# Performance work log

Measured on AMD Instinct MI355X. Metric: run time of the kernel, lower is better.

The kernel has to match this reference:

```python
import jax, jax.numpy as jnp
import numpy as np

G, N, D, K, OUT = 2048, 64, 128, 128, 10  # K*D == input_dim == 16384

def setup_inputs() -> dict:
    key = jax.random.key(0)
    k1, k2, k3, k4, k5 = jax.random.split(key, 5)
    x = jax.random.normal(k1, (G, N, D), dtype=jnp.float32)
    # nn.Linear(node_dim, input_dim/node_dim): weight [K, D], bias [K]
    W_att = jax.random.normal(k2, (K, D), dtype=jnp.float32) * (1.0 / np.sqrt(D))
    b_att = jax.random.normal(k3, (K,), dtype=jnp.float32) * 0.01
    # nn.Linear(input_dim, output_dim): weight [OUT, K*D], bias [OUT]
    W1 = jax.random.normal(k4, (OUT, K * D), dtype=jnp.float32) * (1.0 / np.sqrt(K * D))
    b1 = jax.random.normal(k5, (OUT,), dtype=jnp.float32) * 0.01
    return {"x": x, "W_att": W_att, "b_att": b_att, "W1": W1, "b1": b1}

def reference(x, W_att, b_att, W1, b1):
    # Per-graph gram matrix X^T X : [G, D, D], quantized to 2 decimals
    gram = jnp.einsum('gnd,gne->gde', x, x)
    gram = jnp.round(gram * 100.0) / 100.0
    # attend: Linear(D -> K) applied row-wise to gram -> attn_coef [G, D, K]
    attn = jnp.einsum('gde,ke->gdk', gram, W_att) + b_att
    # attn_weights = attn^T ([G, K, D]); pooled = attn_weights @ gram -> [G, K, D]
    pooled = jnp.einsum('gdk,gde->gke', attn, gram)
    flat = pooled.reshape(x.shape[0], K * D)  # view(input_dim)
    # linear1 (dropout omitted: eval mode)
    return flat @ W1.T + b1
```

## Files before the change

kernel.cpp:

```cpp
#include <hip/hip_runtime.h>

typedef __attribute__((ext_vector_type(8)))  __bf16    bf16x8;
typedef __attribute__((ext_vector_type(4)))  __bf16    bf16x4;
typedef __attribute__((ext_vector_type(16))) float     f32x16;
typedef __attribute__((ext_vector_type(4)))  _Float16  f16x4;
typedef __attribute__((ext_vector_type(2)))  __fp16    h16x2;
typedef __attribute__((ext_vector_type(8)))  __fp16    h16x8;

constexpr int NG  = 2048;
constexpr int NN  = 64;
constexpr int DD  = 128;
constexpr int KK  = 128;
constexpr int OUTD = 10;

__device__ __host__ inline void tileOf(int t, int& ti, int& tj) {
    if (t < 4)      { ti = 0; tj = t;     }
    else if (t < 7) { ti = 1; tj = t - 3; }
    else if (t < 9) { ti = 2; tj = t - 5; }
    else            { ti = 3; tj = 3;     }
}

__device__ inline int xtIdx(int r, int c) { return r * 64  + (c ^ ((r & 7) << 3)); }
__device__ inline int gIdx (int r, int c) { return r * 128 + (c ^ ((r & 15) << 3)); }

#if __has_builtin(__builtin_amdgcn_fdot2)
__device__ __forceinline__ float dot2f(h16x2 a, h16x2 b, float c) {
    return __builtin_amdgcn_fdot2(a, b, c, false);
}
#else
__device__ __forceinline__ float dot2f(h16x2 a, h16x2 b, float c) {
    return c + (float)a[0] * (float)b[0] + (float)a[1] * (float)b[1];
}
#endif

__global__ __launch_bounds__(128)
void precompute_kernel(const float* __restrict__ Wa,
                       const float* __restrict__ b_att,
                       const float* __restrict__ W1,
                       float* __restrict__ A,
                       float* __restrict__ c)
{
    const int o = blockIdx.x >> 7;
    const int f = blockIdx.x & 127;
    const int e = threadIdx.x;
    const float* __restrict__ W1o = W1 + (size_t)o * (KK * DD);

    float acc = 0.f, cacc = 0.f;
    for (int k = 0; k < KK; ++k) {
        const float w1 = W1o[k * DD + e];
        acc  += Wa[k * DD + f] * w1;
        cacc += b_att[k] * w1;
    }
    A[((size_t)o * DD + f) * DD + e] = acc;
    if (f == 0) c[o * DD + e] = cacc;
}

__global__ __launch_bounds__(256)
void pack_kernel(const float* __restrict__ A, _Float16* __restrict__ Sp)
{
    const int b = blockIdx.x;
    const int o = b / 10, t = b - o * 10;
    int ti, tj; tileOf(t, ti, tj);
    const int l  = threadIdx.x & 63;
    const int rq = threadIdx.x >> 6;
    const int e  = tj * 32 + (l & 31);
    const float* __restrict__ Ao = A + (size_t)o * DD * DD;

    f16x4 p;
#pragma unroll
    for (int j = 0; j < 4; ++j) {
        const int f = ti * 32 + j + 8 * rq + 4 * (l >> 5);
        float v;
        if (f < e)       v = Ao[f * DD + e] + Ao[e * DD + f];
        else if (f == e) v = Ao[f * DD + f];
        else             v = 0.f;
        p[j] = (_Float16)v;
    }
    *(f16x4*)&Sp[(size_t)((o * 10 + t) * 64 + l) * 16 + rq * 4] = p;
}

__device__ __forceinline__ void process_graph(
    const float* __restrict__ xg,
    __bf16* __restrict__ XtL, __bf16* __restrict__ GL,
    float (*__restrict__ sp)[DD], float* __restrict__ sOut,
    int tid, int w, int l, int l31, int l5, int extraBase,
    f32x16& hacc0, f32x16& haccX)
{
    {
        const int f = tid & 127, half = tid >> 7;
#pragma unroll
        for (int ch = 0; ch < 2; ++ch) {
            float v[8];
#pragma unroll
            for (int i = 0; i < 8; ++i) v[i] = xg[(half * 16 + ch * 8 + i) * DD + f];
            bf16x8 p;
#pragma unroll
            for (int i = 0; i < 8; ++i) p[i] = (__bf16)v[i];
            *(bf16x8*)&XtL[xtIdx(f, half * 16 + ch * 8)] = p;
        }
    }
    __syncthreads();

    const int ti  = w & 3;
    const int tj0 = (w >> 2) * 2;
    f32x16 acc0, acc1;
#pragma unroll
    for (int i = 0; i < 16; ++i) { acc0[i] = 0.f; acc1[i] = 0.f; }
    {
        const int arow  = ti  * 32 + l31;
        const int brow0 = tj0 * 32 + l31;
#pragma unroll
        for (int ks = 0; ks < 4; ++ks) {
            const int kc = ks * 16 + l5 * 8;
            bf16x8 a  = *(const bf16x8*)&XtL[xtIdx(arow, kc)];
            bf16x8 b0 = *(const bf16x8*)&XtL[xtIdx(brow0, kc)];
            bf16x8 b1 = *(const bf16x8*)&XtL[xtIdx(brow0 + 32, kc)];
            acc0 = __builtin_amdgcn_mfma_f32_32x32x16_bf16(a, b0, acc0, 0, 0, 0);
            acc1 = __builtin_amdgcn_mfma_f32_32x32x16_bf16(a, b1, acc1, 0, 0, 0);
        }
    }
    __syncthreads();

    {
        float sum0 = 0.f, sum1 = 0.f;
#pragma unroll
        for (int tt = 0; tt < 2; ++tt) {
            const int e = (tj0 + tt) * 32 + l31;
#pragma unroll
            for (int g2 = 0; g2 < 4; ++g2) {
                bf16x4 p;
#pragma unroll
                for (int j = 0; j < 4; ++j) {
                    const float av = tt ? acc1[g2 * 4 + j] : acc0[g2 * 4 + j];
                    const float q = rintf(av * 100.f) * 0.01f;
                    p[j] = (__bf16)q;
                    if (tt) sum1 += q; else sum0 += q;
                }
                const int fbase = ti * 32 + g2 * 8 + l5 * 4;
                *(bf16x4*)&GL[gIdx(e, fbase)] = p;
            }
        }
        sp[ti * 2 + l5][tj0 * 32 + l31]       = sum0;
        sp[ti * 2 + l5][(tj0 + 1) * 32 + l31] = sum1;
    }
    __syncthreads();

    if (w == 2 || w == 3) {
        const int e = (w - 2) * 64 + l;
        float s = 0.f;
#pragma unroll
        for (int i = 0; i < 8; ++i) s += sp[i][e];
        sOut[e] = s;
    }

#pragma unroll
    for (int i = 0; i < 16; ++i) hacc0[i] = 0.f;
    {
        int hti, htj; tileOf(w, hti, htj);
        const int ra = hti * 32 + l31, rb = htj * 32 + l31;
#pragma unroll
        for (int ks = 0; ks < 8; ++ks) {
            const int kc = ks * 16 + l5 * 8;
            bf16x8 a = *(const bf16x8*)&GL[gIdx(ra, kc)];
            bf16x8 b = *(const bf16x8*)&GL[gIdx(rb, kc)];
            hacc0 = __builtin_amdgcn_mfma_f32_32x32x16_bf16(a, b, hacc0, 0, 0, 0);
        }
    }
    if (w == extraBase || w == extraBase + 1) {
        int ti1, tj1; tileOf(8 + (w - extraBase), ti1, tj1);
        const int ra = ti1 * 32 + l31, rb = tj1 * 32 + l31;
#pragma unroll
        for (int ks = 0; ks < 8; ++ks) {
            const int kc = ks * 16 + l5 * 8;
            bf16x8 a = *(const bf16x8*)&GL[gIdx(ra, kc)];
            bf16x8 b = *(const bf16x8*)&GL[gIdx(rb, kc)];
            haccX = __builtin_amdgcn_mfma_f32_32x32x16_bf16(a, b, haccX, 0, 0, 0);
        }
    }
    __syncthreads();
}

__global__ __launch_bounds__(512)
void graph_kernel(const float* __restrict__ x,
                  const _Float16* __restrict__ Sp,
                  const float* __restrict__ cg,
                  const float* __restrict__ bias1,
                  float* __restrict__ out)
{
    __shared__ __align__(16) char ldsraw[20 * 512 * 4];
    __shared__ float sp[8][DD];
    __shared__ float sA[DD], sB[DD];

    __bf16* const XtL = (__bf16*)ldsraw;
    __bf16* const GL  = (__bf16*)ldsraw;
    float*  const PP  = (float*)ldsraw;

    const int g0  = blockIdx.x * 2;
    const int g1  = g0 + 1;
    const int tid = threadIdx.x;
    const int w   = tid >> 6;
    const int l   = tid & 63;
    const int l31 = l & 31;
    const int l5  = l >> 5;

    f32x16 hA0, hB0, hX1;
#pragma unroll
    for (int i = 0; i < 16; ++i) hX1[i] = 0.f;

    process_graph(x + (size_t)g0 * NN * DD, XtL, GL, sp, sA,
                  tid, w, l, l31, l5, 6, hA0, hX1);
    process_graph(x + (size_t)g1 * NN * DD, XtL, GL, sp, sB,
                  tid, w, l, l31, l5, 4, hB0, hX1);

    h16x2 hA[8], hB[8], hX[8];
#pragma unroll
    for (int i = 0; i < 8; ++i) {
        hA[i] = __builtin_amdgcn_cvt_pkrtz(hA0[2 * i], hA0[2 * i + 1]);
        hB[i] = __builtin_amdgcn_cvt_pkrtz(hB0[2 * i], hB0[2 * i + 1]);
        hX[i] = __builtin_amdgcn_cvt_pkrtz(hX1[2 * i], hX1[2 * i + 1]);
    }

#pragma unroll
    for (int o = 0; o < OUTD; ++o) {
        const _Float16* __restrict__ spp = Sp + (size_t)((o * 10 + w) * 64 + l) * 16;
        const h16x8 s0 = *(const h16x8*)&spp[0];
        const h16x8 s1 = *(const h16x8*)&spp[8];
        float tA = 0.f, tB = 0.f;
#pragma unroll
        for (int i = 0; i < 4; ++i) {
            const h16x2 p = { s0[2 * i], s0[2 * i + 1] };
            tA = dot2f(p, hA[i], tA);
            tB = dot2f(p, hB[i], tB);
        }
#pragma unroll
        for (int i = 0; i < 4; ++i) {
            const h16x2 p = { s1[2 * i], s1[2 * i + 1] };
            tA = dot2f(p, hA[4 + i], tA);
            tB = dot2f(p, hB[4 + i], tB);
        }
        if (w >= 4) {
            const _Float16* __restrict__ sp2 =
                Sp + (size_t)((o * 10 + 8 + (w & 1)) * 64 + l) * 16;
            const h16x8 e0 = *(const h16x8*)&sp2[0];
            const h16x8 e1 = *(const h16x8*)&sp2[8];
            float tx = 0.f;
#pragma unroll
            for (int i = 0; i < 4; ++i) {
                const h16x2 p = { e0[2 * i], e0[2 * i + 1] };
                tx = dot2f(p, hX[i], tx);
            }
#pragma unroll
            for (int i = 0; i < 4; ++i) {
                const h16x2 p = { e1[2 * i], e1[2 * i + 1] };
                tx = dot2f(p, hX[4 + i], tx);
            }
            if (w >= 6) tA += tx; else tB += tx;
        }
        if (w == 0) {
            tA += cg[o * DD + l] * sA[l] + cg[o * DD + 64 + l] * sA[64 + l];
            tB += cg[o * DD + l] * sB[l] + cg[o * DD + 64 + l] * sB[64 + l];
        }
        PP[o * 512 + tid]        = tA;
        PP[(10 + o) * 512 + tid] = tB;
    }
    __syncthreads();

    for (int p = w; p < 2 * OUTD; p += 8) {
        const float4 q0 = *(const float4*)&PP[p * 512 + l * 8];
        const float4 q1 = *(const float4*)&PP[p * 512 + l * 8 + 4];
        float v = (q0.x + q0.y) + (q0.z + q0.w) + (q1.x + q1.y) + (q1.z + q1.w);
        v += __shfl_down(v, 32, 64);
        v += __shfl_down(v, 16, 64);
        v += __shfl_down(v, 8, 64);
        v += __shfl_down(v, 4, 64);
        v += __shfl_down(v, 2, 64);
        v += __shfl_down(v, 1, 64);
        if (l == 0) {
            const int gg = (p < OUTD) ? g0 : g1;
            const int oo = (p < OUTD) ? p : p - OUTD;
            out[(size_t)gg * OUTD + oo] = v + bias1[oo];
        }
    }
}

extern "C" void kernel_launch(void* const* d_in, const int* in_sizes, int n_in,
                              void* d_out, int out_size, void* d_ws, size_t ws_size,
                              hipStream_t stream)
{
    const float* x     = (const float*)d_in[0];
    const float* Wa    = (const float*)d_in[1];
    const float* b_att = (const float*)d_in[2];
    const float* W1    = (const float*)d_in[3];
    const float* bias1 = (const float*)d_in[4];
    float* out = (float*)d_out;

    float*    A  = (float*)d_ws;
    float*    c  = A + (size_t)OUTD * DD * DD;
    _Float16* Sp = (_Float16*)(c + OUTD * DD);

    precompute_kernel<<<OUTD * DD, 128, 0, stream>>>(Wa, b_att, W1, A, c);
    pack_kernel<<<100, 256, 0, stream>>>(A, Sp);
    graph_kernel<<<NG / 2, 512, 0, stream>>>(x, Sp, c, bias1, out);
}
```

Baseline: 48.63 us.

## Fuse weight precompute and fp16 pack into one tiled LDS kernel

After: 43.23 us. 11.1% less time.

```diff
diff --git a/kernel.cpp b/kernel.cpp
--- a/kernel.cpp
+++ b/kernel.cpp
@@ -33,50 +33,81 @@
 }
 #endif
 
-__global__ __launch_bounds__(128)
-void precompute_kernel(const float* __restrict__ Wa,
-                       const float* __restrict__ b_att,
-                       const float* __restrict__ W1,
-                       float* __restrict__ A,
-                       float* __restrict__ c)
+__global__ __launch_bounds__(256)
+void fused_sp_kernel(const float* __restrict__ Wa,
+                     const float* __restrict__ b_att,
+                     const float* __restrict__ W1,
+                     _Float16* __restrict__ Sp,
+                     float* __restrict__ cgout)
 {
-    const int o = blockIdx.x >> 7;
-    const int f = blockIdx.x & 127;
-    const int e = threadIdx.x;
+    const int blk = blockIdx.x;
+    const int o = blk / 10, t = blk - o * 10;
+    int ti, tj; tileOf(t, ti, tj);
+    const int Fi = ti * 32, Ej = tj * 32;
     const float* __restrict__ W1o = W1 + (size_t)o * (KK * DD);
 
-    float acc = 0.f, cacc = 0.f;
-    for (int k = 0; k < KK; ++k) {
-        const float w1 = W1o[k * DD + e];
-        acc  += Wa[k * DD + f] * w1;
-        cacc += b_att[k] * w1;
-    }
-    A[((size_t)o * DD + f) * DD + e] = acc;
-    if (f == 0) c[o * DD + e] = cacc;
-}
-
-__global__ __launch_bounds__(256)
-void pack_kernel(const float* __restrict__ A, _Float16* __restrict__ Sp)
-{
-    const int b = blockIdx.x;
-    const int o = b / 10, t = b - o * 10;
-    int ti, tj; tileOf(t, ti, tj);
-    const int l  = threadIdx.x & 63;
-    const int rq = threadIdx.x >> 6;
-    const int e  = tj * 32 + (l & 31);
-    const float* __restrict__ Ao = A + (size_t)o * DD * DD;
-
-    f16x4 p;
-#pragma unroll
-    for (int j = 0; j < 4; ++j) {
-        const int f = ti * 32 + j + 8 * rq + 4 * (l >> 5);
-        float v;
-        if (f < e)       v = Ao[f * DD + e] + Ao[e * DD + f];
-        else if (f == e) v = Ao[f * DD + f];
-        else             v = 0.f;
-        p[j] = (_Float16)v;
-    }
-    *(f16x4*)&Sp[(size_t)((o * 10 + t) * 64 + l) * 16 + rq * 4] = p;
+    __shared__ float WaF[KK][32];
+    __shared__ float WaE[KK][32];
+    __shared__ float W1F[KK][32];
+    __shared__ float W1E[KK][32];
+    __shared__ float AFE[32][33];
+    __shared__ float AEF[32][33];
+    __shared__ float bsh[KK];
+
+    const int tid = threadIdx.x;
+
+    for (int r0 = 0; r0 < KK; r0 += 8) {
+        const int r = r0 + (tid >> 5), cc = tid & 31;
+        WaF[r][cc] = Wa[r * DD + Fi + cc];
+        WaE[r][cc] = Wa[r * DD + Ej + cc];
+        W1F[r][cc] = W1o[r * DD + Fi + cc];
+        W1E[r][cc] = W1o[r * DD + Ej + cc];
+    }
+    if (tid < KK) bsh[tid] = b_att[tid];
+    __syncthreads();
+
+    {
+        const int rloc = tid >> 3;
+        const int q    = (tid & 7) * 4;
+        float a0 = 0.f, a1 = 0.f, a2 = 0.f, a3 = 0.f;
+        float b0 = 0.f, b1 = 0.f, b2 = 0.f, b3 = 0.f;
+        for (int k = 0; k < KK; ++k) {
+            const float av = WaF[k][rloc];
+            const float4 wv = *(const float4*)&W1E[k][q];
+            a0 += av * wv.x; a1 += av * wv.y; a2 += av * wv.z; a3 += av * wv.w;
+            const float bv = WaE[k][rloc];
+            const float4 vv = *(const float4*)&W1F[k][q];
+            b0 += bv * vv.x; b1 += bv * vv.y; b2 += bv * vv.z; b3 += bv * vv.w;
+        }
+        AFE[rloc][q] = a0; AFE[rloc][q + 1] = a1; AFE[rloc][q + 2] = a2; AFE[rloc][q + 3] = a3;
+        AEF[rloc][q] = b0; AEF[rloc][q + 1] = b1; AEF[rloc][q + 2] = b2; AEF[rloc][q + 3] = b3;
+    }
+    __syncthreads();
+
+    {
+        const int l  = tid & 63;
+        const int rq = tid >> 6;
+        const int eg = l & 31;
+        const int e  = Ej + eg;
+        f16x4 p;
+#pragma unroll
+        for (int j = 0; j < 4; ++j) {
+            const int fl = j + 8 * rq + 4 * (l >> 5);
+            const int f  = Fi + fl;
+            float v;
+            if (f < e)       v = AFE[fl][eg] + AEF[eg][fl];
+            else if (f == e) v = AFE[fl][eg];
+            else             v = 0.f;
+            p[j] = (_Float16)v;
+        }
+        *(f16x4*)&Sp[(size_t)((o * 10 + t) * 64 + l) * 16 + rq * 4] = p;
+    }
+
+    if (ti == 0 && tid < 32) {
+        float s = 0.f;
+        for (int k = 0; k < KK; ++k) s += bsh[k] * W1E[k][tid];
+        cgout[o * DD + Ej + tid] = s;
+    }
 }
 
 __device__ __forceinline__ void process_graph(
@@ -294,11 +325,9 @@
     const float* bias1 = (const float*)d_in[4];
     float* out = (float*)d_out;
 
-    float*    A  = (float*)d_ws;
-    float*    c  = A + (size_t)OUTD * DD * DD;
-    _Float16* Sp = (_Float16*)(c + OUTD * DD);
-
-    precompute_kernel<<<OUTD * DD, 128, 0, stream>>>(Wa, b_att, W1, A, c);
-    pack_kernel<<<100, 256, 0, stream>>>(A, Sp);
-    graph_kernel<<<NG / 2, 512, 0, stream>>>(x, Sp, c, bias1, out);
-}
+    float*    cg = (float*)d_ws;
+    _Float16* Sp = (_Float16*)(cg + OUTD * DD);
+
+    fused_sp_kernel<<<100, 256, 0, stream>>>(Wa, b_att, W1, Sp, cg);
+    graph_kernel<<<NG / 2, 512, 0, stream>>>(x, Sp, cg, bias1, out);
+}
```
